# Kernel optimization log

Hardware: AMD Instinct MI355X
Metric: run time of the kernel (lower is better)

## Reference

```python
import jax, jax.numpy as jnp
import numpy as np

T_STEPS, B, DX, DH = 512, 64, 1024, 1024


def setup_inputs() -> dict:
    key = jax.random.key(0)
    ks = jax.random.split(key, 8)
    s_in = 1.0 / np.sqrt(DX)
    s_h = 1.0 / np.sqrt(DH)
    return {
        "xs": jax.random.normal(ks[0], (T_STEPS, B, DX), jnp.float32),
        "ms": jax.random.normal(ks[1], (T_STEPS, B, DH), jnp.float32),
        "h0": jnp.zeros((B, DH), jnp.float32),
        "W_ih": jax.random.normal(ks[2], (3 * DH, DX), jnp.float32) * s_in,
        "b_ih": jnp.zeros((3 * DH,), jnp.float32),
        "W_hh": jax.random.normal(ks[3], (3 * DH, DH), jnp.float32) * s_h,
        "b_hh": jnp.zeros((3 * DH,), jnp.float32),
        "W_xh": jax.random.normal(ks[4], (DH, DX), jnp.float32) * s_in,
        "b_xh": jnp.zeros((DH,), jnp.float32),
        "W_r": jax.random.normal(ks[5], (DH, DH), jnp.float32) * s_h,
        "b_r": jnpp if False else jnp.zeros((DH,), jnp.float32),
    }


def reference(xs, ms, h0, W_ih, b_ih, W_hh, b_hh, W_xh, b_xh, W_r, b_r):
    # Precompute all input-side projections in one big GEMM each (same math,
    # just hoisted out of the recurrent loop).
    xg = jnp.einsum('tbd,gd->tbg', xs, W_ih) + b_ih          # [T,B,3*Dh]
    xh = jnp.einsum('tbd,hd->tbh', xs, W_xh) + b_xh          # [T,B,Dh]
    tm = jnp.tanh(ms)                                        # [T,B,Dh]

    def step(h, inp):
        xg_t, xh_t, tm_t = inp
        hg = h @ W_hh.T + b_hh                               # [B,3*Dh]
        gates = jax.nn.sigmoid(xg_t + hg)
        rt, zt, et = jnp.split(gates, 3, axis=-1)
        ht_hat = jnp.tanh(xh_t + (rt * h) @ W_r.T + b_r)
        ht = zt * h + (1.0 - zt) * ht_hat + et * tm_t
        return ht, ht

    h_last, outs = jax.lax.scan(step, h0, (xg, xh, tm))
    return outs, h_last
```

## Files before the change

kernel.cpp:

```cpp
#include <hip/hip_runtime.h>
#include <stdint.h>

#define TSTEPS 512

typedef __attribute__((ext_vector_type(8))) _Float16 half8;
typedef __attribute__((ext_vector_type(4))) _Float16 half4;
typedef __attribute__((ext_vector_type(4))) float f32x4;
typedef __attribute__((ext_vector_type(4))) float float4v;
typedef unsigned long long u64;

static __device__ __forceinline__ float sigm(float x) { return 1.f / (1.f + __expf(-x)); }
static __device__ __forceinline__ float tanh_(float x) {
  x = fminf(15.f, fmaxf(-15.f, x));
  float e = __expf(-2.f * x);
  return (1.f - e) / (1.f + e);
}
static __device__ __forceinline__ half8 ld8(const _Float16* p) { return *(const half8*)p; }
static __device__ __forceinline__ f32x4 MFMA(half8 a, half8 b, f32x4 c) {
  return __builtin_amdgcn_mfma_f32_16x16x32_f16(a, b, c, 0, 0, 0);
}

struct U64x2 { u64 x, y; };
static __device__ __forceinline__ half8 ld_msg16(const u64* p) {
  u64 a = __hip_atomic_load(p,     __ATOMIC_RELAXED, __HIP_MEMORY_SCOPE_AGENT);
  u64 b = __hip_atomic_load(p + 1, __ATOMIC_RELAXED, __HIP_MEMORY_SCOPE_AGENT);
  U64x2 u{a, b};
  return __builtin_bit_cast(half8, u);
}
static __device__ __forceinline__ void st_msg8(u64* p, u64 v) {
  __hip_atomic_store(p, v, __ATOMIC_RELAXED, __HIP_MEMORY_SCOPE_AGENT);
}
static __device__ __forceinline__ void wait_flags(const unsigned* line, unsigned tag) {
  const unsigned* p = line + (threadIdx.x & 31);
  while (!__all(__hip_atomic_load(p, __ATOMIC_RELAXED, __HIP_MEMORY_SCOPE_AGENT) >= tag))
    __builtin_amdgcn_s_sleep(1);
}

__global__ __launch_bounds__(256) void kconv(
    const float* __restrict__ xs, const float* __restrict__ wih,
    const float* __restrict__ wxh, const float* __restrict__ whhf,
    const float* __restrict__ wrf, const float* __restrict__ h0,
    _Float16* __restrict__ xs_h, _Float16* __restrict__ wcat,
    _Float16* __restrict__ whh, _Float16* __restrict__ wr,
    _Float16* __restrict__ hx) {
  const long n1 = 8388608;
  const long n2 = 1048576;
  const long n3 = 786432;
  const long n4 = 262144;
  const long n5 = 16384;
  const long total = n1 + n2 + n3 + n4 + n5;
  for (long i = (long)blockIdx.x * 256 + threadIdx.x; i < total; i += (long)gridDim.x * 256) {
    const float* s; _Float16* d;
    if (i < n1) { s = xs + i * 4; d = xs_h + i * 4; }
    else if (i < n1 + n2) {
      long e = (i - n1) * 4;
      s = (e < 3145728) ? (wih + e) : (wxh + (e - 3145728));
      d = wcat + e;
    } else if (i < n1 + n2 + n3) { long e = (i - n1 - n2) * 4; s = whhf + e; d = whh + e; }
    else if (i < n1 + n2 + n3 + n4) { long e = (i - n1 - n2 - n3) * 4; s = wrf + e; d = wr + e; }
    else { long e = (i - n1 - n2 - n3 - n4) * 4; s = h0 + e; d = hx + e; }
    float4v v = *(const float4v*)s;
    half4 o = { (_Float16)v.x, (_Float16)v.y, (_Float16)v.z, (_Float16)v.w };
    *(half4*)d = o;
  }
}

__global__ __launch_bounds__(256) void kgemm(
    const _Float16* __restrict__ X, const _Float16* __restrict__ W,
    const float* __restrict__ b_ih, const float* __restrict__ b_xh,
    _Float16* __restrict__ C) {
  __shared__ _Float16 As[128 * 40], Bs[128 * 40];
  const int tid = threadIdx.x;
  const int lane = tid & 63;
  const int w = tid >> 6;
  const int wm = (w >> 1) * 64, wn = (w & 1) * 64;
  const int bn = blockIdx.x * 128;
  const int bm = blockIdx.y * 128;
  const int arow = tid >> 2;
  const int kk8 = (tid & 3) * 8;
  const int fr = lane & 15, fq = lane >> 4;
  const f32x4 zero = {0.f, 0.f, 0.f, 0.f};
  f32x4 acc[4][4];
  #pragma unroll
  for (int a = 0; a < 4; a++)
    #pragma unroll
    for (int b = 0; b < 4; b++) acc[a][b] = zero;
  for (int kt = 0; kt < 1024; kt += 32) {
    __syncthreads();
    #pragma unroll
    for (int j = 0; j < 2; j++) {
      int r = j * 64 + arow;
      *(half8*)(As + r * 40 + kk8) = ld8(X + (size_t)(bm + r) * 1024 + kt + kk8);
      *(half8*)(Bs + r * 40 + kk8) = ld8(W + (size_t)(bn + r) * 1024 + kt + kk8);
    }
    __syncthreads();
    half8 af[4], bfr[4];
    #pragma unroll
    for (int i = 0; i < 4; i++) {
      af[i]  = *(const half8*)(As + (wm + i * 16 + fr) * 40 + fq * 8);
      bfr[i] = *(const half8*)(Bs + (wn + i * 16 + fr) * 40 + fq * 8);
    }
    #pragma unroll
    for (int mi = 0; mi < 4; mi++)
      #pragma unroll
      for (int ni = 0; ni < 4; ni++)
        acc[mi][ni] = MFMA(af[mi], bfr[ni], acc[mi][ni]);
  }
  #pragma unroll
  for (int mi = 0; mi < 4; mi++)
    #pragma unroll
    for (int ni = 0; ni < 4; ni++) {
      int col = bn + wn + ni * 16 + fr;
      float bias = (col < 3072) ? b_ih[col] : b_xh[col - 3072];
      #pragma unroll
      for (int r = 0; r < 4; r++) {
        int row = bm + wm + mi * 16 + fq * 4 + r;
        C[(size_t)row * 4096 + col] = (_Float16)(acc[mi][ni][r] + bias);
      }
    }
}

#define TP 272
#define RP 17

__global__ __launch_bounds__(512, 2) void krec(
    const _Float16* __restrict__ xgh, const float* __restrict__ ms,
    const _Float16* __restrict__ whh, const _Float16* __restrict__ wr,
    const float* __restrict__ b_hh, const float* __restrict__ b_r,
    const float* __restrict__ h0,
    _Float16* __restrict__ hx, _Float16* __restrict__ rhx,
    float* __restrict__ out, unsigned* __restrict__ ctr) {
  __shared__ float red[48 * TP];
  __shared__ _Float16 hsh[512];
  const int tid = threadIdx.x;
  const int lane = tid & 63, w = tid >> 6;
  const int fr = lane & 15, fq = lane >> 4;
  const int g = (int)blockIdx.x >> 5;
  const int slot = (int)blockIdx.x & 31;
  const int colbase = slot * 32;
  unsigned* flagA = ctr + (g * 2 + 0) * 32;
  unsigned* flagB = ctr + (g * 2 + 1) * 32;

  half8 wA[6][4], wB[2][4];
  #pragma unroll
  for (int nt = 0; nt < 6; nt++)
    #pragma unroll
    for (int ks = 0; ks < 4; ks++)
      wA[nt][ks] = ld8(whh + (size_t)((nt >> 1) * 1024 + colbase + (nt & 1) * 16 + fr) * 1024
                            + w * 128 + ks * 32 + fq * 8);
  #pragma unroll
  for (int nt = 0; nt < 2; nt++)
    #pragma unroll
    for (int ks = 0; ks < 4; ks++)
      wB[nt][ks] = ld8(wr + (size_t)(colbase + nt * 16 + fr) * 1024
                           + w * 128 + ks * 32 + fq * 8);

  const int b = tid >> 5, cc = tid & 31;
  const int gc = colbase + cc;
  const int gm = g * 16 + b;
  const float bhr = b_hh[gc], bhz = b_hh[1024 + gc], bhe = b_hh[2048 + gc];
  const float brr = b_r[gc];
  float hreg = h0[(size_t)gm * 1024 + gc];

  const u64* hx64  = (const u64*)hx  + (((g * 16 + fr) * 1024 + w * 128 + fq * 8) >> 2);
  const u64* rhx64 = (const u64*)rhx + (((g * 16 + fr) * 1024 + w * 128 + fq * 8) >> 2);
  u64* hpub  = (u64*)hx  + (((g * 16 + (tid >> 3)) * 1024 + colbase + (tid & 7) * 4) >> 2);
  u64* rhpub = (u64*)rhx + (((g * 16 + (tid >> 3)) * 1024 + colbase + (tid & 7) * 4) >> 2);
  const _Float16* hsrc = hsh + (tid >> 3) * 32 + (tid & 7) * 4;

  const f32x4 zero = {0.f, 0.f, 0.f, 0.f};

  float pxr, pxz, pxe, pxh, ptm;
  {
    const _Float16* xp = xgh + (size_t)gm * 4096;
    pxr = (float)xp[gc]; pxz = (float)xp[1024 + gc];
    pxe = (float)xp[2048 + gc]; pxh = (float)xp[3072 + gc];
    ptm = tanh_(ms[(size_t)gm * 1024 + gc]);
  }

  #pragma clang loop unroll(disable)
  for (int t = 0; t < TSTEPS; t++) {
    const int ph = t & 1;
    wait_flags(flagB, (unsigned)t);
    half8 av[4];
    #pragma unroll
    for (int ks = 0; ks < 4; ks++)
      av[ks] = ld_msg16(hx64 + ph * 16384 + ks * 8);
    f32x4 accA[6];
    #pragma unroll
    for (int nt = 0; nt < 6; nt++) accA[nt] = zero;
    #pragma unroll
    for (int ks = 0; ks < 4; ks++)
      #pragma unroll
      for (int nt = 0; nt < 6; nt++)
        accA[nt] = MFMA(av[ks], wA[nt][ks], accA[nt]);
    #pragma unroll
    for (int nt = 0; nt < 6; nt++)
      #pragma unroll
      for (int r = 0; r < 4; r++)
        red[(w * 6 + nt) * TP + (fq * 4 + r) * RP + fr] = accA[nt][r];
    __syncthreads();
    float sr = pxr + bhr, sz = pxz + bhz, se = pxe + bhe;
    {
      const int boff = b * RP + (cc & 15) + (cc >> 4) * TP;
      #pragma unroll
      for (int w8 = 0; w8 < 8; w8++) {
        const float* rp = red + w8 * 6 * TP + boff;
        sr += rp[0]; sz += rp[2 * TP]; se += rp[4 * TP];
      }
    }
    float rg = sigm(sr);
    float zz = sigm(sz), ee = sigm(se);
    hsh[tid] = (_Float16)(rg * hreg);
    __syncthreads();
    if (tid < 128) {
      st_msg8(rhpub + ph * 16384, __builtin_bit_cast(u64, *(const half4*)hsrc));
      asm volatile("s_waitcnt vmcnt(0)" ::: "memory");
    }
    __syncthreads();
    if (tid == 0)
      __hip_atomic_store(flagA + slot, (unsigned)(t + 1),
                         __ATOMIC_RELAXED, __HIP_MEMORY_SCOPE_AGENT);
    float nxr = 0.f, nxz = 0.f, nxe = 0.f, nxh = 0.f, ntm = 0.f;
    if (t + 1 < TSTEPS) {
      const _Float16* xp = xgh + (size_t)((t + 1) * 64 + gm) * 4096;
      nxr = (float)xp[gc]; nxz = (float)xp[1024 + gc];
      nxe = (float)xp[2048 + gc]; nxh = (float)xp[3072 + gc];
      ntm = tanh_(ms[(size_t)(t + 1) * 65536 + gm * 1024 + gc]);
    }
    wait_flags(flagA, (unsigned)(t + 1));

    half8 bv[4];
    #pragma unroll
    for (int ks = 0; ks < 4; ks++)
      bv[ks] = ld_msg16(rhx64 + ph * 16384 + ks * 8);
    f32x4 accB[2];
    #pragma unroll
    for (int nt = 0; nt < 2; nt++) accB[nt] = zero;
    #pragma unroll
    for (int ks = 0; ks < 4; ks++)
      #pragma unroll
      for (int nt = 0; nt < 2; nt++)
        accB[nt] = MFMA(bv[ks], wB[nt][ks], accB[nt]);
    #pragma unroll
    for (int nt = 0; nt < 2; nt++)
      #pragma unroll
      for (int r = 0; r < 4; r++)
        red[(w * 6 + nt) * TP + (fq * 4 + r) * RP + fr] = accB[nt][r];
    __syncthreads();
    float s = pxh + brr;
    {
      const int boff = b * RP + (cc & 15) + (cc >> 4) * TP;
      #pragma unroll
      for (int w8 = 0; w8 < 8; w8++) s += red[w8 * 6 * TP + boff];
    }
    float hh = tanh_(s);
    float hn = zz * hreg + (1.f - zz) * hh + ee * ptm;
    hreg = hn;
    out[(size_t)t * 65536 + gm * 1024 + gc] = hn;
    hsh[tid] = (_Float16)hn;
    __syncthreads();
    if (tid < 128) {
      st_msg8(hpub + (ph ^ 1) * 16384, __builtin_bit_cast(u64, *(const half4*)hsrc));
      asm volatile("s_waitcnt vmcnt(0)" ::: "memory");
    }
    __syncthreads();
    if (tid == 0)
      __hip_atomic_store(flagB + slot, (unsigned)(t + 1),
                         __ATOMIC_RELAXED, __HIP_MEMORY_SCOPE_AGENT);
    pxr = nxr; pxz = nxz; pxe = nxe; pxh = nxh; ptm = ntm;
  }
  out[(size_t)TSTEPS * 65536 + gm * 1024 + gc] = hreg;
}

extern "C" void kernel_launch(void* const* d_in, const int* in_sizes, int n_in,
                              void* d_out, int out_size, void* d_ws, size_t ws_size,
                              hipStream_t stream) {
  const float* xs   = (const float*)d_in[0];
  const float* ms   = (const float*)d_in[1];
  const float* h0   = (const float*)d_in[2];
  const float* W_ih = (const float*)d_in[3];
  const float* b_ih = (const float*)d_in[4];
  const float* W_hh = (const float*)d_in[5];
  const float* b_hh = (const float*)d_in[6];
  const float* W_xh = (const float*)d_in[7];
  const float* b_xh = (const float*)d_in[8];
  const float* W_r  = (const float*)d_in[9];
  const float* b_r  = (const float*)d_in[10];

  char* ws = (char*)d_ws;
  size_t off = 0;
  _Float16* xs_h = (_Float16*)(ws + off); off += 67108864;
  _Float16* wcat = (_Float16*)(ws + off); off += 8388608;
  _Float16* whh  = (_Float16*)(ws + off); off += 6291456;
  _Float16* wr   = (_Float16*)(ws + off); off += 2097152;
  _Float16* xgh  = (_Float16*)(ws + off); off += 268435456;
  _Float16* hx   = (_Float16*)(ws + off); off += 262144;
  _Float16* rhx  = (_Float16*)(ws + off); off += 262144;
  unsigned* ctr  = (unsigned*)(ws + off); off += 1024;

  hipMemsetAsync(ctr, 0, 1024, stream);
  kconv<<<2048, 256, 0, stream>>>(xs, W_ih, W_xh, W_hh, W_r, h0,
                                  xs_h, wcat, whh, wr, hx);
  kgemm<<<dim3(32, 256), 256, 0, stream>>>(xs_h, wcat, b_ih, b_xh, xgh);
  krec<<<128, 512, 0, stream>>>(xgh, ms, whh, wr, b_hh, b_r, h0,
                                hx, rhx, (float*)d_out, ctr);
}
```

Baseline: 4.480 ms.

## Replace flag-based inter-block sync with tagged self-validating message words

The recurrent kernel no longer publishes h and r*h then signals a separate per-slot flag. Each 64-bit message word now carries two fp16 values plus a step tag in the upper half. Consumers spin directly on the data words until every tag matches, which removes the store-drain waits, two block barriers and the separate flag round trip per half-step. The cost is double the message traffic, since half of each word is tag, and polling on 16 words per lane. Output stores are also made nontemporal.

```diff
diff --git a/kernel.cpp b/kernel.cpp
--- a/kernel.cpp
+++ b/kernel.cpp
@@ -5,8 +5,10 @@
 
 typedef __attribute__((ext_vector_type(8))) _Float16 half8;
 typedef __attribute__((ext_vector_type(4))) _Float16 half4;
+typedef __attribute__((ext_vector_type(2))) _Float16 half2v;
 typedef __attribute__((ext_vector_type(4))) float f32x4;
 typedef __attribute__((ext_vector_type(4))) float float4v;
+typedef __attribute__((ext_vector_type(4))) int i32x4;
 typedef unsigned long long u64;
 
 static __device__ __forceinline__ float sigm(float x) { return 1.f / (1.f + __expf(-x)); }
@@ -20,20 +22,11 @@
   return __builtin_amdgcn_mfma_f32_16x16x32_f16(a, b, c, 0, 0, 0);
 }
 
-struct U64x2 { u64 x, y; };
-static __device__ __forceinline__ half8 ld_msg16(const u64* p) {
-  u64 a = __hip_atomic_load(p,     __ATOMIC_RELAXED, __HIP_MEMORY_SCOPE_AGENT);
-  u64 b = __hip_atomic_load(p + 1, __ATOMIC_RELAXED, __HIP_MEMORY_SCOPE_AGENT);
-  U64x2 u{a, b};
-  return __builtin_bit_cast(half8, u);
-}
-static __device__ __forceinline__ void st_msg8(u64* p, u64 v) {
+static __device__ __forceinline__ u64 ld_msg(const u64* p) {
+  return __hip_atomic_load(p, __ATOMIC_RELAXED, __HIP_MEMORY_SCOPE_AGENT);
+}
+static __device__ __forceinline__ void st_msg(u64* p, u64 v) {
   __hip_atomic_store(p, v, __ATOMIC_RELAXED, __HIP_MEMORY_SCOPE_AGENT);
-}
-static __device__ __forceinline__ void wait_flags(const unsigned* line, unsigned tag) {
-  const unsigned* p = line + (threadIdx.x & 31);
-  while (!__all(__hip_atomic_load(p, __ATOMIC_RELAXED, __HIP_MEMORY_SCOPE_AGENT) >= tag))
-    __builtin_amdgcn_s_sleep(1);
 }
 
 __global__ __launch_bounds__(256) void kconv(
@@ -42,26 +35,38 @@
     const float* __restrict__ wrf, const float* __restrict__ h0,
     _Float16* __restrict__ xs_h, _Float16* __restrict__ wcat,
     _Float16* __restrict__ whh, _Float16* __restrict__ wr,
-    _Float16* __restrict__ hx) {
+    u64* __restrict__ hmsg, u64* __restrict__ rhmsg) {
   const long n1 = 8388608;
   const long n2 = 1048576;
   const long n3 = 786432;
   const long n4 = 262144;
-  const long n5 = 16384;
-  const long total = n1 + n2 + n3 + n4 + n5;
+  const long b4 = n1 + n2 + n3 + n4;
+  const long n5 = 32768;
+  const long n6 = 32768;
+  const long total = b4 + n5 + n6;
   for (long i = (long)blockIdx.x * 256 + threadIdx.x; i < total; i += (long)gridDim.x * 256) {
-    const float* s; _Float16* d;
-    if (i < n1) { s = xs + i * 4; d = xs_h + i * 4; }
-    else if (i < n1 + n2) {
-      long e = (i - n1) * 4;
-      s = (e < 3145728) ? (wih + e) : (wxh + (e - 3145728));
-      d = wcat + e;
-    } else if (i < n1 + n2 + n3) { long e = (i - n1 - n2) * 4; s = whhf + e; d = whh + e; }
-    else if (i < n1 + n2 + n3 + n4) { long e = (i - n1 - n2 - n3) * 4; s = wrf + e; d = wr + e; }
-    else { long e = (i - n1 - n2 - n3 - n4) * 4; s = h0 + e; d = hx + e; }
-    float4v v = *(const float4v*)s;
-    half4 o = { (_Float16)v.x, (_Float16)v.y, (_Float16)v.z, (_Float16)v.w };
-    *(half4*)d = o;
+    if (i < b4) {
+      const float* s; _Float16* d;
+      if (i < n1) { s = xs + i * 4; d = xs_h + i * 4; }
+      else if (i < n1 + n2) {
+        long e = (i - n1) * 4;
+        s = (e < 3145728) ? (wih + e) : (wxh + (e - 3145728));
+        d = wcat + e;
+      } else if (i < n1 + n2 + n3) { long e = (i - n1 - n2) * 4; s = whhf + e; d = whh + e; }
+      else { long e = (i - n1 - n2 - n3) * 4; s = wrf + e; d = wr + e; }
+      float4v v = *(const float4v*)s;
+      half4 o = { (_Float16)v.x, (_Float16)v.y, (_Float16)v.z, (_Float16)v.w };
+      *(half4*)d = o;
+    } else if (i < b4 + n5) {
+      long e = i - b4;
+      int g = (int)(e >> 13), rem = (int)(e & 8191);
+      int row = rem >> 9, pr = rem & 511;
+      const float* hp = h0 + (size_t)(g * 16 + row) * 1024 + 2 * pr;
+      half2v h2 = { (_Float16)hp[0], (_Float16)hp[1] };
+      hmsg[e] = (u64)(unsigned)__builtin_bit_cast(unsigned, h2);
+    } else {
+      rhmsg[i - b4 - n5] = 0xFFFFFFFF00000000ull;
+    }
   }
 }
 
@@ -128,8 +133,8 @@
     const _Float16* __restrict__ whh, const _Float16* __restrict__ wr,
     const float* __restrict__ b_hh, const float* __restrict__ b_r,
     const float* __restrict__ h0,
-    _Float16* __restrict__ hx, _Float16* __restrict__ rhx,
-    float* __restrict__ out, unsigned* __restrict__ ctr) {
+    u64* __restrict__ hmsg, u64* __restrict__ rhmsg,
+    float* __restrict__ out) {
   __shared__ float red[48 * TP];
   __shared__ _Float16 hsh[512];
   const int tid = threadIdx.x;
@@ -138,8 +143,6 @@
   const int g = (int)blockIdx.x >> 5;
   const int slot = (int)blockIdx.x & 31;
   const int colbase = slot * 32;
-  unsigned* flagA = ctr + (g * 2 + 0) * 32;
-  unsigned* flagB = ctr + (g * 2 + 1) * 32;
 
   half8 wA[6][4], wB[2][4];
   #pragma unroll
@@ -162,11 +165,12 @@
   const float brr = b_r[gc];
   float hreg = h0[(size_t)gm * 1024 + gc];
 
-  const u64* hx64  = (const u64*)hx  + (((g * 16 + fr) * 1024 + w * 128 + fq * 8) >> 2);
-  const u64* rhx64 = (const u64*)rhx + (((g * 16 + fr) * 1024 + w * 128 + fq * 8) >> 2);
-  u64* hpub  = (u64*)hx  + (((g * 16 + (tid >> 3)) * 1024 + colbase + (tid & 7) * 4) >> 2);
-  u64* rhpub = (u64*)rhx + (((g * 16 + (tid >> 3)) * 1024 + colbase + (tid & 7) * 4) >> 2);
-  const _Float16* hsrc = hsh + (tid >> 3) * 32 + (tid & 7) * 4;
+  const u64* hcons = hmsg  + g * 8192 + fr * 512 + w * 64 + fq * 4;
+  const u64* rcons = rhmsg + g * 8192 + fr * 512 + w * 64 + fq * 4;
+  const int prow = tid >> 4, pp = tid & 15;
+  u64* hprod = hmsg  + g * 8192 + prow * 512 + slot * 16 + pp;
+  u64* rprod = rhmsg + g * 8192 + prow * 512 + slot * 16 + pp;
+  const unsigned* hsrc = (const unsigned*)(hsh + prow * 32 + 2 * pp);
 
   const f32x4 zero = {0.f, 0.f, 0.f, 0.f};
 
@@ -180,12 +184,29 @@
 
   #pragma clang loop unroll(disable)
   for (int t = 0; t < TSTEPS; t++) {
-    const int ph = t & 1;
-    wait_flags(flagB, (unsigned)t);
+    u64 m[16];
+    {
+      const unsigned tagv = (unsigned)t;
+      for (;;) {
+        bool ok = true;
+        #pragma unroll
+        for (int ks = 0; ks < 4; ks++)
+          #pragma unroll
+          for (int q = 0; q < 4; q++)
+            m[ks * 4 + q] = ld_msg(hcons + ks * 16 + q);
+        #pragma unroll
+        for (int i = 0; i < 16; i++) ok &= ((unsigned)(m[i] >> 32) == tagv);
+        if (ok) break;
+        __builtin_amdgcn_s_sleep(1);
+      }
+    }
     half8 av[4];
     #pragma unroll
-    for (int ks = 0; ks < 4; ks++)
-      av[ks] = ld_msg16(hx64 + ph * 16384 + ks * 8);
+    for (int ks = 0; ks < 4; ks++) {
+      i32x4 u = { (int)(unsigned)m[ks * 4 + 0], (int)(unsigned)m[ks * 4 + 1],
+                  (int)(unsigned)m[ks * 4 + 2], (int)(unsigned)m[ks * 4 + 3] };
+      av[ks] = __builtin_bit_cast(half8, u);
+    }
     f32x4 accA[6];
     #pragma unroll
     for (int nt = 0; nt < 6; nt++) accA[nt] = zero;
@@ -213,14 +234,8 @@
     float zz = sigm(sz), ee = sigm(se);
     hsh[tid] = (_Float16)(rg * hreg);
     __syncthreads();
-    if (tid < 128) {
-      st_msg8(rhpub + ph * 16384, __builtin_bit_cast(u64, *(const half4*)hsrc));
-      asm volatile("s_waitcnt vmcnt(0)" ::: "memory");
-    }
-    __syncthreads();
-    if (tid == 0)
-      __hip_atomic_store(flagA + slot, (unsigned)(t + 1),
-                         __ATOMIC_RELAXED, __HIP_MEMORY_SCOPE_AGENT);
+    if (tid < 256)
+      st_msg(rprod, ((u64)(unsigned)(t + 1) << 32) | (u64)*hsrc);
     float nxr = 0.f, nxz = 0.f, nxe = 0.f, nxh = 0.f, ntm = 0.f;
     if (t + 1 < TSTEPS) {
       const _Float16* xp = xgh + (size_t)((t + 1) * 64 + gm) * 4096;
@@ -228,12 +243,29 @@
       nxe = (float)xp[2048 + gc]; nxh = (float)xp[3072 + gc];
       ntm = tanh_(ms[(size_t)(t + 1) * 65536 + gm * 1024 + gc]);
     }
-    wait_flags(flagA, (unsigned)(t + 1));
-
+
+    {
+      const unsigned tagv = (unsigned)(t + 1);
+      for (;;) {
+        bool ok = true;
+        #pragma unroll
+        for (int ks = 0; ks < 4; ks++)
+          #pragma unroll
+          for (int q = 0; q < 4; q++)
+            m[ks * 4 + q] = ld_msg(rcons + ks * 16 + q);
+        #pragma unroll
+        for (int i = 0; i < 16; i++) ok &= ((unsigned)(m[i] >> 32) == tagv);
+        if (ok) break;
+        __builtin_amdgcn_s_sleep(1);
+      }
+    }
     half8 bv[4];
     #pragma unroll
-    for (int ks = 0; ks < 4; ks++)
-      bv[ks] = ld_msg16(rhx64 + ph * 16384 + ks * 8);
+    for (int ks = 0; ks < 4; ks++) {
+      i32x4 u = { (int)(unsigned)m[ks * 4 + 0], (int)(unsigned)m[ks * 4 + 1],
+                  (int)(unsigned)m[ks * 4 + 2], (int)(unsigned)m[ks * 4 + 3] };
+      bv[ks] = __builtin_bit_cast(half8, u);
+    }
     f32x4 accB[2];
     #pragma unroll
     for (int nt = 0; nt < 2; nt++) accB[nt] = zero;
@@ -257,17 +289,11 @@
     float hh = tanh_(s);
     float hn = zz * hreg + (1.f - zz) * hh + ee * ptm;
     hreg = hn;
-    out[(size_t)t * 65536 + gm * 1024 + gc] = hn;
+    __builtin_nontemporal_store(hn, out + (size_t)t * 65536 + gm * 1024 + gc);
     hsh[tid] = (_Float16)hn;
     __syncthreads();
-    if (tid < 128) {
-      st_msg8(hpub + (ph ^ 1) * 16384, __builtin_bit_cast(u64, *(const half4*)hsrc));
-      asm volatile("s_waitcnt vmcnt(0)" ::: "memory");
-    }
-    __syncthreads();
-    if (tid == 0)
-      __hip_atomic_store(flagB + slot, (unsigned)(t + 1),
-                         __ATOMIC_RELAXED, __HIP_MEMORY_SCOPE_AGENT);
+    if (tid < 256)
+      st_msg(hprod, ((u64)(unsigned)(t + 1) << 32) | (u64)*hsrc);
     pxr = nxr; pxz = nxz; pxe = nxe; pxh = nxh; ptm = ntm;
   }
   out[(size_t)TSTEPS * 65536 + gm * 1024 + gc] = hreg;
@@ -295,14 +321,12 @@
   _Float16* whh  = (_Float16*)(ws + off); off += 6291456;
   _Float16* wr   = (_Float16*)(ws + off); off += 2097152;
   _Float16* xgh  = (_Float16*)(ws + off); off += 268435456;
-  _Float16* hx   = (_Float16*)(ws + off); off += 262144;
-  _Float16* rhx  = (_Float16*)(ws + off); off += 262144;
-  unsigned* ctr  = (unsigned*)(ws + off); off += 1024;
-
-  hipMemsetAsync(ctr, 0, 1024, stream);
+  u64* hmsg  = (u64*)(ws + off); off += 262144;
+  u64* rhmsg = (u64*)(ws + off); off += 262144;
+
   kconv<<<2048, 256, 0, stream>>>(xs, W_ih, W_xh, W_hh, W_r, h0,
-                                  xs_h, wcat, whh, wr, hx);
+                                  xs_h, wcat, whh, wr, hmsg, rhmsg);
   kgemm<<<dim3(32, 256), 256, 0, stream>>>(xs_h, wcat, b_ih, b_xh, xgh);
   krec<<<128, 512, 0, stream>>>(xgh, ms, whh, wr, b_hh, b_r, h0,
-                                hx, rhx, (float*)d_out, ctr);
-}
+                                hmsg, rhmsg, (float*)d_out);
+}
```

New measurement: 6.031 ms. +34.6%, slower.
